# Kernel tuning notes

Hardware: AMD Instinct MI355X
Metric: run time of the kernel (lower is better)

Reference implementation:

```python
import jax, jax.numpy as jnp
import numpy as np
from itertools import combinations

A = 4          # anchor_points
K = 16         # neighbor_num
INTRA = A * (A - 1) // 2   # 6
CH = INTRA * 2 + A * A     # 28 = generator channels
B, N, S = 1, 8192, 4096
CIN, COUT = 64, 128


def cdist(x):
    # pairwise euclidean distances [B,N,N], zero-safe sqrt (zero grad at d=0)
    sq = jnp.sum(x * x, -1)
    d2 = sq[:, :, None] + sq[:, None, :] - 2.0 * jnp.einsum('bnc,bmc->bnm', x, x)
    d2 = jnp.maximum(d2, 0.0)
    m = d2 > 0
    return jnp.where(m, jnp.sqrt(jnp.where(m, d2, 1.0)), 0.0)


def index_points(points, idx):
    # points [B,N,...], idx [B,*] -> [B,*,...]
    return jax.vmap(lambda p, i: p[i])(points, idx)


def index_points_dists(dists, i1, i2):
    # dists [B,N,N]; result[b,...] = dists[b, i1[b,...], i2[b,...]]
    i1, i2 = jnp.broadcast_arrays(i1, i2)
    return jax.vmap(lambda d, a, b: d[a, b])(dists, i1, i2)


def generator(xyz):
    # RotationInvariantDistFea.forward(xyz, concat_raw_relative_fea=True)
    D = cdist(xyz)
    neg_nd, ni = jax.lax.top_k(-D, K)   # K >= A; smallest-K, sorted ascending
    nd = -neg_nd
    ai = ni[:, :, :A]
    # intra-anchor dists: dists to anchors 1..A-1 plus pairwise dists among them
    subs = [index_points_dists(D, ai[:, :, pi], ai[:, :, pj])[:, :, None]
            for pi, pj in combinations(range(1, A), 2)]
    intra = jnp.concatenate([nd[:, :, 1:A]] + subs, axis=2)  # [B,P,6]
    # inter-anchor dists: center anchors x neighbor anchors -> [B,P,K,A*A]
    nai = index_points(ai, ni)                                # [B,P,K,A]
    inter = index_points_dists(D, ai[:, :, None, :, None],
                               nai[:, :, :, None, :]).reshape(D.shape[0], D.shape[1], K, A * A)
    center = jnp.broadcast_to(intra[:, :, None, :], (intra.shape[0], intra.shape[1], K, INTRA))
    rf = jnp.concatenate([center, index_points(intra, ni), inter], axis=3)  # [B,P,K,28]
    return rf, ni, D


def mlp(x, W, b, g, be, act):
    # Linear + BatchNorm1d (training mode: stats over batch*points) + optional leaky_relu(0.2)
    y = x @ W + b
    mu = jnp.mean(y, (0, 1))
    var = jnp.var(y, (0, 1))
    y = (y - mu) * jax.lax.rsqrt(var + 1e-5) * g + be
    return jax.nn.leaky_relu(y, 0.2) if act else y


def forward(xyz, feature, sample_indexes, Ww, bw, gw, betaw, Wb, bb, gb, betab, Wo, bo, go, betao):
    rf_before, ni_before, D_before = generator(xyz)
    intra_before = rf_before[:, :, 0, :INTRA]
    xyz_s = index_points(xyz, sample_indexes)
    feat = index_points(feature, sample_indexes)
    intra_before = index_points(intra_before, sample_indexes)
    rf_after, ni_after, _ = generator(xyz_s)
    intra_after = rf_after[:, :, 0, :INTRA]
    a_before = index_points(ni_before[:, :, :A], sample_indexes)                  # [B,S,A]
    a_after = jax.vmap(lambda s, a: s[a])(sample_indexes, ni_after[:, :, :A])     # map to global idx
    inter = index_points_dists(D_before, a_before[:, :, :, None],
                               a_after[:, :, None, :]).reshape(B, S, A * A)
    adf = jnp.concatenate([intra_before, intra_after, inter], axis=2)             # [B,S,28]
    w = mlp(adf, Ww, bw, gw, betaw, False)
    bia = mlp(adf, Wb, bb, gb, betab, False)
    feat = jax.nn.leaky_relu(feat * w + bia, 0.2)
    feat = jnp.concatenate([feat, adf], axis=2)                                   # [B,S,92]
    feat = mlp(feat, Wo, bo, go, betao, True)                                     # [B,S,128]
    return xyz_s, feat, rf_after, ni_after


def setup_inputs():
    key = jax.random.key(0)
    ks = jax.random.split(key, 8)
    xyz = jax.random.normal(ks[0], (B, N, 3), jnp.float32)
    feature = jax.random.normal(ks[1], (B, N, CIN), jnp.float32)
    sample_indexes = jnp.stack([jax.random.permutation(jax.random.fold_in(ks[2], i), N)[:S]
                                for i in range(B)]).astype(jnp.int32)

    def lin(k, cin, cout):
        k1, k2 = jax.random.split(k)
        W = jax.random.normal(k1, (cin, cout), jnp.float32) / np.float32(np.sqrt(cin))
        b = jax.random.normal(k2, (cout,), jnp.float32) * 0.01
        return W, b, jnp.ones((cout,), jnp.float32), jnp.zeros((cout,), jnp.float32)

    Ww, bw, gw, betaw = lin(ks[5], CH, CIN)
    Wb, bb, gb, betab = lin(ks[6], CH, CIN)
    Wo, bo, go, betao = lin(ks[7], CH + CIN, COUT)
    return dict(xyz=xyz, feature=feature, sample_indexes=sample_indexes,
                Ww=Ww, bw=bw, gw=gw, betaw=betaw,
                Wb=Wb, bb=bb, gb=gb, betab=betab,
                Wo=Wo, bo=bo, go=go, betao=betao)


def reference(xyz, feature, sample_indexes, Ww, bw, gw, betaw, Wb, bb, gb, betab, Wo, bo, go, betao):
    return forward(xyz, feature, sample_indexes, Ww, bw, gw, betaw, Wb, bb, gb, betab, Wo, bo, go, betao)
```

## Files before the change

### kernel.cpp

```cpp
#include <hip/hip_runtime.h>
#include <hip/hip_bf16.h>
#include <math.h>

#define N_PTS 8192
#define S_PTS 4096
typedef unsigned long long u64;
typedef unsigned u32;

__device__ __forceinline__ float d2_f32_gram(const float4 a, const float4 b) {
    float dot = __fadd_rn(__fadd_rn(__fmul_rn(a.x, b.x), __fmul_rn(a.y, b.y)),
                          __fmul_rn(a.z, b.z));
    float d2 = __fsub_rn(__fadd_rn(a.w, b.w), __fmul_rn(2.0f, dot));
    return fmaxf(d2, 0.0f);
}

__device__ __forceinline__ float pair_dist_f(const float4 a, const float4 b) {
    float d2 = d2_f32_gram(a, b);
    return d2 > 0.0f ? __fsqrt_rn(d2) : 0.0f;
}

__global__ __launch_bounds__(256) void stage_kernel(
        const float* __restrict__ xyz, const int* __restrict__ sidx,
        float4* __restrict__ cb, float4* __restrict__ ca,
        float* __restrict__ out_xyz_s) {
    int i = blockIdx.x * blockDim.x + threadIdx.x;
    if (i < N_PTS) {
        float x = xyz[i * 3 + 0], y = xyz[i * 3 + 1], z = xyz[i * 3 + 2];
        float sq = __fadd_rn(__fadd_rn(__fmul_rn(x, x), __fmul_rn(y, y)),
                             __fmul_rn(z, z));
        cb[i] = make_float4(x, y, z, sq);
    }
    if (i < S_PTS) {
        int si = sidx[i];
        float x = xyz[si * 3 + 0], y = xyz[si * 3 + 1], z = xyz[si * 3 + 2];
        float sq = __fadd_rn(__fadd_rn(__fmul_rn(x, x), __fmul_rn(y, y)),
                             __fmul_rn(z, z));
        ca[i] = make_float4(x, y, z, sq);
        out_xyz_s[i * 3 + 0] = x;
        out_xyz_s[i * 3 + 1] = y;
        out_xyz_s[i * 3 + 2] = z;
    }
}


template <int KOUT, int ITERS>
__device__ u64 knn_full_ladder(const float4 q, const float4* __restrict__ cand,
                               int lane) {
    u32 Lk[KOUT], Li[KOUT];
#pragma unroll
    for (int j = 0; j < KOUT; ++j) { Lk[j] = 0xFFFFFFFFu; Li[j] = 0xFFFFFFFFu; }
    int c = lane;
    for (int tt = 0; tt < ITERS; ++tt, c += 64) {
        float d2 = d2_f32_gram(q, cand[c]);
        float Df = d2 > 0.0f ? __fsqrt_rn(d2) : 0.0f;
        u32 kb = __float_as_uint(Df);
        if (kb < Lk[KOUT - 1]) {
#pragma unroll
            for (int j = KOUT - 1; j >= 1; --j) {
                bool up = kb < Lk[j - 1], ins = kb < Lk[j];
                Lk[j] = up ? Lk[j - 1] : (ins ? kb : Lk[j]);
                Li[j] = up ? Li[j - 1] : (ins ? (u32)c : Li[j]);
            }
            bool i0 = kb < Lk[0];
            Lk[0] = i0 ? kb : Lk[0];
            Li[0] = i0 ? (u32)c : Li[0];
        }
    }
    u64 Lu[KOUT];
#pragma unroll
    for (int j = 0; j < KOUT; ++j) Lu[j] = ((u64)Lk[j] << 32) | (u64)Li[j];
    u64 res = ~0ull;
#pragma unroll
    for (int r = 0; r < KOUT; ++r) {
        u64 m = Lu[0];
#pragma unroll
        for (int off = 32; off >= 1; off >>= 1) {
            u64 o = __shfl_xor(m, off, 64);
            m = (o < m) ? o : m;
        }
        if (lane == r) res = m;
        if (Lu[0] == m) {
#pragma unroll
            for (int j = 0; j < KOUT - 1; ++j) Lu[j] = Lu[j + 1];
            Lu[KOUT - 1] = ~0ull;
        }
    }
    return res;
}

template <int K, int NC>
__device__ u64 final_select(const float4 qq, const float4* __restrict__ cand,
                            const u64* bufq, u32 cnt, int lane) {
    if (cnt <= 64u) {
        u64 v = (lane < (int)cnt) ? bufq[lane] : ~0ull;
#pragma unroll
        for (int k = 2; k <= 64; k <<= 1) {
#pragma unroll
            for (int j2 = k >> 1; j2 >= 1; j2 >>= 1) {
                u64 o = __shfl_xor(v, j2, 64);
                bool keepMin = (((lane & j2) == 0) == ((lane & k) == 0));
                bool less = o < v;
                v = keepMin ? (less ? o : v) : (less ? v : o);
            }
        }
        return v;
    } else if (cnt <= 256u) {
        u64 L0 = ~0ull, L1 = ~0ull, L2 = ~0ull, L3 = ~0ull;
        for (u32 mm = lane; mm < cnt; mm += 64) {
            u64 kk = bufq[mm];
            if (kk < L3) {
                if (kk < L1) {
                    L3 = L2; L2 = L1;
                    if (kk < L0) { L1 = L0; L0 = kk; } else L1 = kk;
                } else {
                    if (kk < L2) { L3 = L2; L2 = kk; } else L3 = kk;
                }
            }
        }
        u64 res = ~0ull;
#pragma unroll
        for (int r = 0; r < K; ++r) {
            u64 mr = L0;
#pragma unroll
            for (int off = 32; off >= 1; off >>= 1) {
                u64 o = __shfl_xor(mr, off, 64);
                mr = (o < mr) ? o : mr;
            }
            if (lane == r) res = mr;
            if (L0 == mr) { L0 = L1; L1 = L2; L2 = L3; L3 = ~0ull; }
        }
        return res;
    }
    return knn_full_ladder<K, NC / 64>(qq, cand, lane);
}

template <int J, int K, int NC, int Q>
__device__ __forceinline__ u64 knn_selectq(
        const float4* qs, const float4* __restrict__ cand, int t,
        u32* mins, u64* buf, u32* shm) {
    int lane = t & 63, wid = t >> 6;
    u32 d2b[Q][J];
    u32 m[Q];
#pragma unroll
    for (int qi = 0; qi < Q; ++qi) m[qi] = 0xFFFFFFFFu;
#pragma unroll
    for (int j = 0; j < J; ++j) {
        float4 c = cand[t + 256 * j];
#pragma unroll
        for (int qi = 0; qi < Q; ++qi) {
            u32 b = __float_as_uint(d2_f32_gram(qs[qi], c));
            d2b[qi][j] = b;
            m[qi] = b < m[qi] ? b : m[qi];
        }
    }
#pragma unroll
    for (int qi = 0; qi < Q; ++qi) mins[qi * 256 + t] = m[qi];
    __syncthreads();
    if (wid < Q) {
        const u32* mq = mins + wid * 256;
        u32 v = mq[lane];
        u32 v2 = mq[lane + 64];  v = v2 < v ? v2 : v;
        v2 = mq[lane + 128];     v = v2 < v ? v2 : v;
        v2 = mq[lane + 192];     v = v2 < v ? v2 : v;
#pragma unroll
        for (int k = 2; k <= 64; k <<= 1) {
#pragma unroll
            for (int j2 = k >> 1; j2 >= 1; j2 >>= 1) {
                u32 o = __shfl_xor(v, j2, 64);
                bool keepMin = (((lane & j2) == 0) == ((lane & k) == 0));
                bool less = o < v;
                v = keepMin ? (less ? o : v) : (less ? v : o);
            }
        }
        if (lane == K - 1) shm[wid] = v;
    }
    __syncthreads();
    u32 tau[Q], c[Q], x[Q];
#pragma unroll
    for (int qi = 0; qi < Q; ++qi) {
        tau[qi] = shm[qi];
        u32 cc = 0;
#pragma unroll
        for (int j = 0; j < J; ++j) cc += (d2b[qi][j] <= tau[qi]) ? 1u : 0u;
        c[qi] = cc;
        u32 xx = cc;
#pragma unroll
        for (int off = 1; off < 64; off <<= 1) {
            u32 y = __shfl_up(xx, off, 64);
            if (lane >= off) xx += y;
        }
        x[qi] = xx;
        if (lane == 63) shm[Q + qi * 4 + wid] = xx;
    }
    __syncthreads();
    u32 cnt[Q];
#pragma unroll
    for (int qi = 0; qi < Q; ++qi) {
        u32 base = x[qi] - c[qi];
        for (int w = 0; w < wid; ++w) base += shm[Q + qi * 4 + w];
        cnt[qi] = shm[Q + qi * 4 + 0] + shm[Q + qi * 4 + 1] +
                  shm[Q + qi * 4 + 2] + shm[Q + qi * 4 + 3];
        if (cnt[qi] <= 256u) {
            u32 off = base;
#pragma unroll
            for (int j = 0; j < J; ++j) {
                if (d2b[qi][j] <= tau[qi]) {
                    float d2 = __uint_as_float(d2b[qi][j]);
                    float D = d2 > 0.0f ? __fsqrt_rn(d2) : 0.0f;
                    buf[qi * 256 + off++] = ((u64)__float_as_uint(D) << 32) |
                                            (u64)(u32)(t + 256 * j);
                }
            }
        }
    }
    __syncthreads();
    u64 res = ~0ull;
#pragma unroll
    for (int qi = 0; qi < Q; ++qi)
        if (wid == qi)
            res = final_select<K, NC>(qs[qi], cand, buf + qi * 256, cnt[qi], lane);
    return res;
}

__global__ __launch_bounds__(256, 4) void knn_kernel(
        const float4* __restrict__ cb, const float4* __restrict__ ca,
        const int* __restrict__ sidx,
        int* __restrict__ a_before, float* __restrict__ intra_before,
        int* __restrict__ ni_i, float* __restrict__ intra_after,
        float* __restrict__ out_ni) {
    __shared__ u32 mins[4 * 256];
    __shared__ u64 buf[4 * 256];
    __shared__ u32 shm[24];
    int t = threadIdx.x, lane = t & 63, wid = t >> 6;
    int bid = blockIdx.x;
    if (bid < S_PTS / 4) {
        int s0 = bid * 4;
        float4 qs[4];
#pragma unroll
        for (int qi = 0; qi < 4; ++qi) qs[qi] = ca[s0 + qi];
        u64 res = knn_selectq<16, 16, 4096, 4>(qs, ca, t, mins, buf, shm);
        if (wid < 4) {
            int s = s0 + wid;
            int idx = (int)(res & 0xffffffffull);
            if (lane < 16) {
                ni_i[s * 16 + lane] = idx;
                out_ni[s * 16 + lane] = (float)idx;
            }
            if (lane >= 1 && lane < 4)
                intra_after[s * 6 + (lane - 1)] =
                    __uint_as_float((u32)(res >> 32));
            int i1 = __shfl(idx, 1, 64);
            int i2 = __shfl(idx, 2, 64);
            int i3 = __shfl(idx, 3, 64);
            if (lane < 3) {
                int pa = (lane == 2) ? i2 : i1;
                int pb = (lane == 0) ? i2 : i3;
                intra_after[s * 6 + 3 + lane] = pair_dist_f(ca[pa], ca[pb]);
            }
        }
    } else {
        int s0 = (bid - S_PTS / 4) * 2;
        float4 qs[2];
        qs[0] = cb[sidx[s0]];
        qs[1] = cb[sidx[s0 + 1]];
        u64 res = knn_selectq<32, 4, 8192, 2>(qs, cb, t, mins, buf, shm);
        if (wid < 2) {
            int s = s0 + wid;
            int idx = (int)(res & 0xffffffffull);
            if (lane < 4) a_before[s * 4 + lane] = idx;
            if (lane >= 1 && lane < 4)
                intra_before[s * 6 + (lane - 1)] =
                    __uint_as_float((u32)(res >> 32));
            int i1 = __shfl(idx, 1, 64);
            int i2 = __shfl(idx, 2, 64);
            int i3 = __shfl(idx, 3, 64);
            if (lane < 3) {
                int pa = (lane == 2) ? i2 : i1;
                int pb = (lane == 0) ? i2 : i3;
                intra_before[s * 6 + 3 + lane] = pair_dist_f(cb[pa], cb[pb]);
            }
        }
    }
}

__global__ __launch_bounds__(256) void assemble_kernel(
        const float4* __restrict__ ca, const float4* __restrict__ cb,
        const int* __restrict__ ni_i, const float* __restrict__ intra_after,
        const int* __restrict__ a_before, const float* __restrict__ intra_before,
        const int* __restrict__ sidx,
        float* __restrict__ out_rf, float* __restrict__ adf) {
    __shared__ int s_ni[4][16];
    __shared__ float s_rf[4][16 * 28];
    __shared__ float s_ia[4][8];
    int t = threadIdx.x, wid = t >> 6, lane = t & 63;
    int s = blockIdx.x * 4 + wid;
    if (lane < 16) s_ni[wid][lane] = ni_i[s * 16 + lane];
    if (lane < 6) s_ia[wid][lane] = intra_after[s * 6 + lane];
    __syncthreads();

    int k = lane >> 2, qq = lane & 3;
    int nai_q = ni_i[s_ni[wid][k] * 16 + qq];
    float4 pq = ca[nai_q];
#pragma unroll
    for (int p = 0; p < 4; ++p) {
        float4 pp = ca[s_ni[wid][p]];
        s_rf[wid][k * 28 + 12 + p * 4 + qq] = pair_dist_f(pp, pq);
    }
    for (int idx = lane; idx < 16 * 12; idx += 64) {
        int kk = idx / 12, c = idx % 12;
        float v = (c < 6) ? s_ia[wid][c] : intra_after[s_ni[wid][kk] * 6 + (c - 6)];
        s_rf[wid][kk * 28 + c] = v;
    }
    if (lane < 16) {
        int p = lane >> 2, q2 = lane & 3;
        int ib = a_before[s * 4 + p];
        int ia = sidx[s_ni[wid][q2]];
        adf[s * 28 + 12 + lane] = pair_dist_f(cb[ib], cb[ia]);
    } else if (lane >= 32 && lane < 38) {
        adf[s * 28 + (lane - 32)] = intra_before[s * 6 + (lane - 32)];
    } else if (lane >= 40 && lane < 46) {
        adf[s * 28 + 6 + (lane - 40)] = s_ia[wid][lane - 40];
    }
    __syncthreads();
    const int base = s * 16 * 28;
    for (int idx = lane; idx < 16 * 28; idx += 64) out_rf[base + idx] = s_rf[wid][idx];
}

__global__ __launch_bounds__(256) void mlp1_kernel(
        const float* __restrict__ adf,
        const float* __restrict__ Ww, const float* __restrict__ bw,
        const float* __restrict__ Wb, const float* __restrict__ bb,
        float* __restrict__ y_wb) {
    __shared__ float sW[28 * 128];
    __shared__ float sb[128];
    __shared__ float sA[32 * 28];
    int t = threadIdx.x;
    for (int i = t; i < 28 * 128; i += 256) {
        int k = i >> 7, c = i & 127;
        sW[i] = (c < 64) ? Ww[k * 64 + c] : Wb[k * 64 + (c - 64)];
    }
    if (t < 128) sb[t] = (t < 64) ? bw[t] : bb[t - 64];
    int s0 = blockIdx.x * 32;
    for (int i = t; i < 32 * 28; i += 256) sA[i] = adf[s0 * 28 + i];
    __syncthreads();
    int sl = t >> 3, grp = t & 7;
    int s = s0 + sl;
    float acc[16];
#pragma unroll
    for (int k = 0; k < 16; ++k) acc[k] = sb[grp * 16 + k];
    for (int k2 = 0; k2 < 28; ++k2) {
        float a = sA[sl * 28 + k2];
#pragma unroll
        for (int k = 0; k < 16; ++k)
            acc[k] = fmaf(a, sW[k2 * 128 + grp * 16 + k], acc[k]);
    }
#pragma unroll
    for (int k = 0; k < 16; ++k) y_wb[(grp * 16 + k) * 4096 + s] = acc[k];
}

__global__ __launch_bounds__(256) void stats_kernel(
        const float* __restrict__ y,
        const float* __restrict__ g0, const float* __restrict__ be0,
        const float* __restrict__ g1, const float* __restrict__ be1, int csplit,
        float* __restrict__ scale, float* __restrict__ shift) {
    int c = blockIdx.x;
    const float* p = y + c * 4096;
    float s1 = 0.0f, s2 = 0.0f;
    for (int i = threadIdx.x; i < 4096; i += 256) {
        float v = p[i];
        s1 += v;
        s2 = fmaf(v, v, s2);
    }
    __shared__ float l1[256], l2[256];
    l1[threadIdx.x] = s1;
    l2[threadIdx.x] = s2;
    __syncthreads();
    for (int off = 128; off; off >>= 1) {
        if (threadIdx.x < off) {
            l1[threadIdx.x] += l1[threadIdx.x + off];
            l2[threadIdx.x] += l2[threadIdx.x + off];
        }
        __syncthreads();
    }
    if (threadIdx.x == 0) {
        float mean = l1[0] * (1.0f / 4096.0f);
        float var = l2[0] * (1.0f / 4096.0f) - mean * mean;
        float g = (c < csplit) ? g0[c] : g1[c - csplit];
        float be = (c < csplit) ? be0[c] : be1[c - csplit];
        float sc = g / sqrtf(var + 1e-5f);
        scale[c] = sc;
        shift[c] = be - mean * sc;
    }
}

__global__ __launch_bounds__(256) void mlp2_kernel(
        const float* __restrict__ y_wb,
        const float* __restrict__ scale1, const float* __restrict__ shift1,
        const float* __restrict__ feature, const int* __restrict__ sidx,
        const float* __restrict__ adf,
        const float* __restrict__ Wo, const float* __restrict__ bo,
        float* __restrict__ y_o) {
    __shared__ float sW[92 * 128];
    __shared__ float t2[16 * 129];
    __shared__ float scat[16 * 92];
    int t = threadIdx.x;
    int s0 = blockIdx.x * 16;
    for (int i = t; i < 92 * 128; i += 256) sW[i] = Wo[i];
    for (int i = t; i < 16 * 128; i += 256) {
        int row = i & 15, c = i >> 4;
        t2[row * 129 + c] = fmaf(y_wb[c * 4096 + s0 + row], scale1[c], shift1[c]);
    }
    __syncthreads();
    for (int rr = 0; rr < 16; rr += 4) {
        int r = rr + (t >> 6);
        int c = t & 63;
        int si = sidx[s0 + r];
        float f = feature[si * 64 + c];
        float v = fmaf(f, t2[r * 129 + c], t2[r * 129 + 64 + c]);
        scat[r * 92 + c] = v >= 0.0f ? v : 0.2f * v;
    }
    for (int i = t; i < 16 * 28; i += 256) {
        int row = i / 28, k = i % 28;
        scat[row * 92 + 64 + k] = adf[(s0 + row) * 28 + k];
    }
    __syncthreads();
    int r = t >> 4, cg = t & 15;
    float acc[8];
#pragma unroll
    for (int j = 0; j < 8; ++j) acc[j] = bo[cg * 8 + j];
    for (int c = 0; c < 92; ++c) {
        float a = scat[r * 92 + c];
#pragma unroll
        for (int j = 0; j < 8; ++j)
            acc[j] = fmaf(a, sW[c * 128 + cg * 8 + j], acc[j]);
    }
    int s = s0 + r;
#pragma unroll
    for (int j = 0; j < 8; ++j) y_o[(cg * 8 + j) * 4096 + s] = acc[j];
}

__global__ __launch_bounds__(256) void stats_final_kernel(
        const float* __restrict__ y_o,
        const float* __restrict__ go, const float* __restrict__ betao,
        float* __restrict__ out_feat) {
    int c = blockIdx.x;
    const float* p = y_o + c * 4096;
    float s1 = 0.0f, s2 = 0.0f;
    for (int i = threadIdx.x; i < 4096; i += 256) {
        float v = p[i];
        s1 += v;
        s2 = fmaf(v, v, s2);
    }
    __shared__ float l1[256], l2[256];
    __shared__ float s_sc, s_sh;
    l1[threadIdx.x] = s1;
    l2[threadIdx.x] = s2;
    __syncthreads();
    for (int off = 128; off; off >>= 1) {
        if (threadIdx.x < off) {
            l1[threadIdx.x] += l1[threadIdx.x + off];
            l2[threadIdx.x] += l2[threadIdx.x + off];
        }
        __syncthreads();
    }
    if (threadIdx.x == 0) {
        float mean = l1[0] * (1.0f / 4096.0f);
        float var = l2[0] * (1.0f / 4096.0f) - mean * mean;
        float sc = go[c] / sqrtf(var + 1e-5f);
        s_sc = sc;
        s_sh = betao[c] - mean * sc;
    }
    __syncthreads();
    float sc = s_sc, sh = s_sh;
    for (int i = threadIdx.x; i < 4096; i += 256) {
        float v = fmaf(p[i], sc, sh);
        v = v >= 0.0f ? v : 0.2f * v;
        out_feat[i * 128 + c] = v;
    }
}

extern "C" void kernel_launch(void* const* d_in, const int* in_sizes, int n_in,
                              void* d_out, int out_size, void* d_ws, size_t ws_size,
                              hipStream_t stream) {
    const float* xyz = (const float*)d_in[0];
    const float* feature = (const float*)d_in[1];
    const int* sidx = (const int*)d_in[2];
    const float* Ww = (const float*)d_in[3];
    const float* bw = (const float*)d_in[4];
    const float* gw = (const float*)d_in[5];
    const float* betaw = (const float*)d_in[6];
    const float* Wb = (const float*)d_in[7];
    const float* bb = (const float*)d_in[8];
    const float* gb = (const float*)d_in[9];
    const float* betab = (const float*)d_in[10];
    const float* Wo = (const float*)d_in[11];
    const float* bo = (const float*)d_in[12];
    const float* go = (const float*)d_in[13];
    const float* betao = (const float*)d_in[14];

    float* out = (float*)d_out;
    float* out_xyz = out;
    float* out_feat = out + 12288;
    float* out_rf = out + 12288 + 524288;
    float* out_ni = out + 12288 + 524288 + 1835008;

    float* ws = (float*)d_ws;
    float4* cb = (float4*)ws;
    float4* ca = (float4*)(ws + 32768);
    int* a_before = (int*)(ws + 49152);
    float* intra_before = ws + 65536;
    int* ni_i = (int*)(ws + 90112);
    float* intra_after = ws + 155648;
    float* adf = ws + 180224;
    float* y_wb = ws + 294912;
    float* y_o = ws + 819200;
    float* scale1 = ws + 1343488;
    float* shift1 = ws + 1343616;

    stage_kernel<<<32, 256, 0, stream>>>(xyz, sidx, cb, ca, out_xyz);
    knn_kernel<<<S_PTS / 4 + S_PTS / 2, 256, 0, stream>>>(
        cb, ca, sidx, a_before, intra_before, ni_i, intra_after, out_ni);
    assemble_kernel<<<1024, 256, 0, stream>>>(ca, cb, ni_i, intra_after, a_before,
                                              intra_before, sidx, out_rf, adf);
    mlp1_kernel<<<128, 256, 0, stream>>>(adf, Ww, bw, Wb, bb, y_wb);
    stats_kernel<<<128, 256, 0, stream>>>(y_wb, gw, betaw, gb, betab, 64, scale1, shift1);
    mlp2_kernel<<<256, 256, 0, stream>>>(y_wb, scale1, shift1, feature, sidx, adf, Wo, bo, y_o);
    stats_final_kernel<<<128, 256, 0, stream>>>(y_o, go, betao, out_feat);
}
```

Measured before the change: 166.4 us.

## Register top-4 KNN for 8192-point branch and fold BN stats into MLP kernels

```diff
diff --git a/kernel.cpp b/kernel.cpp
--- a/kernel.cpp
+++ b/kernel.cpp
@@ -228,12 +228,13 @@
         int* __restrict__ a_before, float* __restrict__ intra_before,
         int* __restrict__ ni_i, float* __restrict__ intra_after,
         float* __restrict__ out_ni) {
-    __shared__ u32 mins[4 * 256];
-    __shared__ u64 buf[4 * 256];
+    __shared__ u64 big[4096];
     __shared__ u32 shm[24];
     int t = threadIdx.x, lane = t & 63, wid = t >> 6;
     int bid = blockIdx.x;
     if (bid < S_PTS / 4) {
+        u32* mins = (u32*)big;
+        u64* buf = big + 1024;
         int s0 = bid * 4;
         float4 qs[4];
 #pragma unroll
@@ -259,13 +260,68 @@
             }
         }
     } else {
-        int s0 = (bid - S_PTS / 4) * 2;
-        float4 qs[2];
-        qs[0] = cb[sidx[s0]];
-        qs[1] = cb[sidx[s0 + 1]];
-        u64 res = knn_selectq<32, 4, 8192, 2>(qs, cb, t, mins, buf, shm);
-        if (wid < 2) {
-            int s = s0 + wid;
+        int s0 = (bid - S_PTS / 4) * 4;
+        float4 qs[4];
+#pragma unroll
+        for (int qi = 0; qi < 4; ++qi) qs[qi] = cb[sidx[s0 + qi]];
+        u64 Lu[4][4];
+#pragma unroll
+        for (int qi = 0; qi < 4; ++qi)
+#pragma unroll
+            for (int r = 0; r < 4; ++r) Lu[qi][r] = ~0ull;
+#pragma unroll 4
+        for (int j = 0; j < 32; ++j) {
+            float4 c4 = cb[t + 256 * j];
+            u32 ci = (u32)(t + 256 * j);
+#pragma unroll
+            for (int qi = 0; qi < 4; ++qi) {
+                float d2 = d2_f32_gram(qs[qi], c4);
+                float Df = d2 > 0.0f ? __fsqrt_rn(d2) : 0.0f;
+                u64 kk = ((u64)__float_as_uint(Df) << 32) | (u64)ci;
+                if (kk < Lu[qi][3]) {
+                    if (kk < Lu[qi][1]) {
+                        Lu[qi][3] = Lu[qi][2]; Lu[qi][2] = Lu[qi][1];
+                        if (kk < Lu[qi][0]) { Lu[qi][1] = Lu[qi][0]; Lu[qi][0] = kk; }
+                        else Lu[qi][1] = kk;
+                    } else {
+                        if (kk < Lu[qi][2]) { Lu[qi][3] = Lu[qi][2]; Lu[qi][2] = kk; }
+                        else Lu[qi][3] = kk;
+                    }
+                }
+            }
+        }
+#pragma unroll
+        for (int qi = 0; qi < 4; ++qi)
+#pragma unroll
+            for (int r = 0; r < 4; ++r) big[qi * 1024 + t * 4 + r] = Lu[qi][r];
+        __syncthreads();
+        {
+            int qi = wid;
+            u64 M0 = ~0ull, M1 = ~0ull, M2 = ~0ull, M3 = ~0ull;
+            for (int i = lane; i < 1024; i += 64) {
+                u64 kk = big[qi * 1024 + i];
+                if (kk < M3) {
+                    if (kk < M1) {
+                        M3 = M2; M2 = M1;
+                        if (kk < M0) { M1 = M0; M0 = kk; } else M1 = kk;
+                    } else {
+                        if (kk < M2) { M3 = M2; M2 = kk; } else M3 = kk;
+                    }
+                }
+            }
+            u64 res = ~0ull;
+#pragma unroll
+            for (int r = 0; r < 4; ++r) {
+                u64 mr = M0;
+#pragma unroll
+                for (int off = 32; off >= 1; off >>= 1) {
+                    u64 o = __shfl_xor(mr, off, 64);
+                    mr = (o < mr) ? o : mr;
+                }
+                if (lane == r) res = mr;
+                if (M0 == mr) { M0 = M1; M1 = M2; M2 = M3; M3 = ~0ull; }
+            }
+            int s = s0 + qi;
             int idx = (int)(res & 0xffffffffull);
             if (lane < 4) a_before[s * 4 + lane] = idx;
             if (lane >= 1 && lane < 4)
@@ -330,10 +386,12 @@
         const float* __restrict__ adf,
         const float* __restrict__ Ww, const float* __restrict__ bw,
         const float* __restrict__ Wb, const float* __restrict__ bb,
-        float* __restrict__ y_wb) {
+        float* __restrict__ y_wb,
+        float* __restrict__ part1, float* __restrict__ part2) {
     __shared__ float sW[28 * 128];
     __shared__ float sb[128];
     __shared__ float sA[32 * 28];
+    __shared__ float red[32][128];
     int t = threadIdx.x;
     for (int i = t; i < 28 * 128; i += 256) {
         int k = i >> 7, c = i & 127;
@@ -355,47 +413,29 @@
             acc[k] = fmaf(a, sW[k2 * 128 + grp * 16 + k], acc[k]);
     }
 #pragma unroll
-    for (int k = 0; k < 16; ++k) y_wb[(grp * 16 + k) * 4096 + s] = acc[k];
-}
-
-__global__ __launch_bounds__(256) void stats_kernel(
-        const float* __restrict__ y,
-        const float* __restrict__ g0, const float* __restrict__ be0,
-        const float* __restrict__ g1, const float* __restrict__ be1, int csplit,
-        float* __restrict__ scale, float* __restrict__ shift) {
-    int c = blockIdx.x;
-    const float* p = y + c * 4096;
-    float s1 = 0.0f, s2 = 0.0f;
-    for (int i = threadIdx.x; i < 4096; i += 256) {
-        float v = p[i];
-        s1 += v;
-        s2 = fmaf(v, v, s2);
-    }
-    __shared__ float l1[256], l2[256];
-    l1[threadIdx.x] = s1;
-    l2[threadIdx.x] = s2;
-    __syncthreads();
-    for (int off = 128; off; off >>= 1) {
-        if (threadIdx.x < off) {
-            l1[threadIdx.x] += l1[threadIdx.x + off];
-            l2[threadIdx.x] += l2[threadIdx.x + off];
-        }
-        __syncthreads();
-    }
-    if (threadIdx.x == 0) {
-        float mean = l1[0] * (1.0f / 4096.0f);
-        float var = l2[0] * (1.0f / 4096.0f) - mean * mean;
-        float g = (c < csplit) ? g0[c] : g1[c - csplit];
-        float be = (c < csplit) ? be0[c] : be1[c - csplit];
-        float sc = g / sqrtf(var + 1e-5f);
-        scale[c] = sc;
-        shift[c] = be - mean * sc;
+    for (int k = 0; k < 16; ++k) {
+        y_wb[(grp * 16 + k) * 4096 + s] = acc[k];
+        red[sl][grp * 16 + k] = acc[k];
+    }
+    __syncthreads();
+    if (t < 128) {
+        float s1 = 0.0f, s2 = 0.0f;
+#pragma unroll 8
+        for (int r = 0; r < 32; ++r) {
+            float v = red[r][t];
+            s1 += v;
+            s2 = fmaf(v, v, s2);
+        }
+        part1[blockIdx.x * 128 + t] = s1;
+        part2[blockIdx.x * 128 + t] = s2;
     }
 }
 
 __global__ __launch_bounds__(256) void mlp2_kernel(
         const float* __restrict__ y_wb,
-        const float* __restrict__ scale1, const float* __restrict__ shift1,
+        const float* __restrict__ part1, const float* __restrict__ part2,
+        const float* __restrict__ gw, const float* __restrict__ betaw,
+        const float* __restrict__ gb, const float* __restrict__ betab,
         const float* __restrict__ feature, const int* __restrict__ sidx,
         const float* __restrict__ adf,
         const float* __restrict__ Wo, const float* __restrict__ bo,
@@ -403,12 +443,28 @@
     __shared__ float sW[92 * 128];
     __shared__ float t2[16 * 129];
     __shared__ float scat[16 * 92];
+    __shared__ float s_sc[128], s_sh[128];
     int t = threadIdx.x;
     int s0 = blockIdx.x * 16;
+    if (t < 128) {
+        float s1 = 0.0f, s2 = 0.0f;
+        for (int b = 0; b < 128; ++b) {
+            s1 += part1[b * 128 + t];
+            s2 += part2[b * 128 + t];
+        }
+        float mean = s1 * (1.0f / 4096.0f);
+        float var = s2 * (1.0f / 4096.0f) - mean * mean;
+        float g = (t < 64) ? gw[t] : gb[t - 64];
+        float be = (t < 64) ? betaw[t] : betab[t - 64];
+        float sc = g / sqrtf(var + 1e-5f);
+        s_sc[t] = sc;
+        s_sh[t] = be - mean * sc;
+    }
     for (int i = t; i < 92 * 128; i += 256) sW[i] = Wo[i];
+    __syncthreads();
     for (int i = t; i < 16 * 128; i += 256) {
         int row = i & 15, c = i >> 4;
-        t2[row * 129 + c] = fmaf(y_wb[c * 4096 + s0 + row], scale1[c], shift1[c]);
+        t2[row * 129 + c] = fmaf(y_wb[c * 4096 + s0 + row], s_sc[c], s_sh[c]);
     }
     __syncthreads();
     for (int rr = 0; rr < 16; rr += 4) {
@@ -514,16 +570,16 @@
     float* adf = ws + 180224;
     float* y_wb = ws + 294912;
     float* y_o = ws + 819200;
-    float* scale1 = ws + 1343488;
-    float* shift1 = ws + 1343616;
+    float* part1 = ws + 1343488;
+    float* part2 = ws + 1359872;
 
     stage_kernel<<<32, 256, 0, stream>>>(xyz, sidx, cb, ca, out_xyz);
-    knn_kernel<<<S_PTS / 4 + S_PTS / 2, 256, 0, stream>>>(
+    knn_kernel<<<S_PTS / 4 + S_PTS / 4, 256, 0, stream>>>(
         cb, ca, sidx, a_before, intra_before, ni_i, intra_after, out_ni);
     assemble_kernel<<<1024, 256, 0, stream>>>(ca, cb, ni_i, intra_after, a_before,
                                               intra_before, sidx, out_rf, adf);
-    mlp1_kernel<<<128, 256, 0, stream>>>(adf, Ww, bw, Wb, bb, y_wb);
-    stats_kernel<<<128, 256, 0, stream>>>(y_wb, gw, betaw, gb, betab, 64, scale1, shift1);
-    mlp2_kernel<<<256, 256, 0, stream>>>(y_wb, scale1, shift1, feature, sidx, adf, Wo, bo, y_o);
+    mlp1_kernel<<<128, 256, 0, stream>>>(adf, Ww, bw, Wb, bb, y_wb, part1, part2);
+    mlp2_kernel<<<256, 256, 0, stream>>>(y_wb, part1, part2, gw, betaw, gb, betab,
+                                         feature, sidx, adf, Wo, bo, y_o);
     stats_final_kernel<<<128, 256, 0, stream>>>(y_o, go, betao, out_feat);
 }
```

Result: slower. 187.9 us (+13.0%).
